# Kernel tuning notes

Measured on AMD Instinct MI355X. Metric: run time of the kernel, lower is better.

## Reference

```python
import jax, jax.numpy as jnp
import numpy as np

EMBED = 128   # embed_dim
HEADS = 8
POINTS = 4
H_SP, W_SP = 51, 102   # hardcoded spatial_shapes in __init__
BEV = 100              # bev_res
HRES = 50              # height_res


def _make_ref_points():
    """Exact numpy replica of the spherical grid built in __init__."""
    eps = 1e-6
    x = np.linspace(-71 / 2, 71 / 2, BEV)
    y = np.linspace(-71 / 2, 71 / 2, BEV)
    z = np.linspace(-50 / 2, 50 / 2, HRES)
    gx, gy, gz = np.meshgrid(x, y, z, indexing='ij')
    phi = np.sign(gy + eps) * np.arccos(gx / (np.sqrt(gx ** 2 + gy ** 2) + eps))
    theta = np.arccos(gz / (np.sqrt(gx ** 2 + gy ** 2 + gz ** 2) + eps))
    phi = 2 * np.pi - phi
    phi[phi > 2 * np.pi] -= 2 * np.pi
    col = phi / (2 * np.pi)   # grd_col_cross
    row = theta / np.pi       # grd_row_cross
    ref = np.stack([col, row], axis=-1)              # (BEV, BEV, HRES, 2)
    ref = ref.transpose(2, 0, 1, 3).reshape(HRES, BEV * BEV, 2)
    return jnp.asarray(ref, dtype=jnp.float32)


def setup_inputs() -> dict:
    key = jax.random.key(0)
    ks = jax.random.split(key, 12)
    d = EMBED
    s = 0.02
    return {
        'query': jax.random.normal(ks[0], (1, BEV * BEV, d), jnp.float32),
        'value': jax.random.normal(ks[1], (1, H_SP * W_SP, d), jnp.float32),
        'ref_points': _make_ref_points(),
        'W_off': jax.random.normal(ks[2], (d, HEADS * POINTS * 2), jnp.float32) * s,
        'b_off': jax.random.normal(ks[3], (HEADS * POINTS * 2,), jnp.float32) * s,
        'W_attn': jax.random.normal(ks[4], (d, HEADS * POINTS), jnp.float32) * s,
        'b_attn': jax.random.normal(ks[5], (HEADS * POINTS,), jnp.float32) * s,
        'W_val': jax.random.normal(ks[6], (d, d), jnp.float32) * s,
        'b_val': jax.random.normal(ks[7], (d,), jnp.float32) * s,
        'W_out': jax.random.normal(ks[8], (d, d), jnp.float32) * s,
        'b_out': jax.random.normal(ks[9], (d,), jnp.float32) * s,
        'W_proj': jax.random.normal(ks[10], (d, 1), jnp.float32) * s,
        'b_proj': jax.random.normal(ks[11], (1,), jnp.float32) * s,
    }


def _bilinear_sample(vflat, loc):
    """grid_sample(bilinear, zero padding, align_corners=False).
    vflat: (B, H*W, hd) value maps; loc: (B, N, 2) normalized [0,1] (x,y)."""
    px = loc[..., 0] * W_SP - 0.5
    py = loc[..., 1] * H_SP - 0.5
    x0 = jnp.floor(px)
    y0 = jnp.floor(py)
    dx = (px - x0)[..., None]
    dy = (py - y0)[..., None]
    x0i = x0.astype(jnp.int32)
    y0i = y0.astype(jnp.int32)

    def gather(xi, yi):
        valid = (xi >= 0) & (xi < W_SP) & (yi >= 0) & (yi < H_SP)
        idx = jnp.clip(yi, 0, H_SP - 1) * W_SP + jnp.clip(xi, 0, W_SP - 1)
        v = jnp.take_along_axis(vflat, idx[..., None], axis=1)  # (B, N, hd)
        return v * valid[..., None].astype(vflat.dtype)

    v00 = gather(x0i, y0i)
    v01 = gather(x0i + 1, y0i)
    v10 = gather(x0i, y0i + 1)
    v11 = gather(x0i + 1, y0i + 1)
    return (v00 * (1 - dx) * (1 - dy) + v01 * dx * (1 - dy)
            + v10 * (1 - dx) * dy + v11 * dx * dy)


def reference(query, value, ref_points, W_off, b_off, W_attn, b_attn,
              W_val, b_val, W_out, b_out, W_proj, b_proj):
    bs, nq, d = query.shape
    hd = d // HEADS
    L = ref_points.shape[0]

    # query-dependent MSDA projections (identical across height levels)
    offsets = (query @ W_off + b_off).reshape(bs, nq, HEADS, POINTS, 2)
    aw = jax.nn.softmax((query @ W_attn + b_attn).reshape(bs, nq, HEADS, POINTS), axis=-1)
    awt = aw.transpose(0, 2, 1, 3)                              # (bs, heads, nq, points)
    v = (value @ W_val + b_val).reshape(bs, -1, HEADS, hd)
    vflat = v.transpose(0, 2, 1, 3).reshape(bs * HEADS, H_SP * W_SP, hd)
    norm = jnp.asarray([W_SP, H_SP], dtype=query.dtype)         # offset_normalizer [W, H]

    def per_level(ref):  # ref: (nq, 2) -> MSDA output with its internal residual
        loc = ref[None, :, None, None, :] + offsets / norm      # (bs, nq, heads, pts, 2)
        loc = loc.transpose(0, 2, 1, 3, 4).reshape(bs * HEADS, nq * POINTS, 2)
        samp = _bilinear_sample(vflat, loc).reshape(bs, HEADS, nq, POINTS, hd)
        out = jnp.einsum('bhnp,bhnpd->bnhd', awt, samp).reshape(bs, nq, d)
        return out @ W_out + b_out + query                      # mmcv MSDA adds identity

    grd = jax.vmap(per_level)(ref_points)                       # (L, bs, nq, d)
    grd_3d = grd.transpose(1, 2, 0, 3).reshape(bs, BEV, BEV, L, d)
    weights = jax.nn.softmax(grd_3d @ W_proj + b_proj, axis=3)  # (bs, BEV, BEV, L, 1)
    max_height_index = jnp.argmax(weights, axis=3)              # (bs, BEV, BEV, 1)
    grd_bev = (weights * grd_3d).sum(axis=3)                    # (bs, BEV, BEV, d)
    return grd_bev.reshape(bs, nq, d) + query, max_height_index
```

## Files before the change

### kernel.cpp

```cpp
#include <hip/hip_runtime.h>
#include <math.h>

#define EMBED   128
#define NHEADS  8
#define NPOINTS 4
#define HD      16
#define HSP     51
#define WSP     102
#define NPIX    (HSP * WSP)
#define NQ      10000
#define NLVL    50

#define GRID_A ((NPIX + 7) / 8)
#define GRID_B (NQ / 8)

__global__ __launch_bounds__(256) void k_prep(
    const float* __restrict__ value,
    const float* __restrict__ Wv,
    const float* __restrict__ bv,
    const float* __restrict__ query,
    const float* __restrict__ Woff,
    const float* __restrict__ boff,
    const float* __restrict__ Wattn,
    const float* __restrict__ battn,
    const float* __restrict__ Wout,
    const float* __restrict__ Wproj,
    float* __restrict__ vout,
    float* __restrict__ off_out,
    float* __restrict__ aw_out,
    float* __restrict__ u_out) {
    const int b = blockIdx.x;
    const int t = threadIdx.x;
    __shared__ float srow[8][EMBED];

    if (b < GRID_A) {
        const int p   = t >> 5;
        const int s   = t & 31;
        const int pix = b * 8 + p;
        const int pl  = min(pix, NPIX - 1);
        *(float4*)&srow[p][s * 4] =
            *(const float4*)(value + (size_t)pl * EMBED + s * 4);
        __syncthreads();
        float4 acc = *(const float4*)(bv + s * 4);
        const float* vr = srow[p];
        const float* wp = Wv + s * 4;
#pragma unroll 8
        for (int k = 0; k < EMBED; ++k) {
            const float qv = vr[k];
            const float4 w4 = *(const float4*)(wp + (size_t)k * EMBED);
            acc.x = fmaf(qv, w4.x, acc.x);
            acc.y = fmaf(qv, w4.y, acc.y);
            acc.z = fmaf(qv, w4.z, acc.z);
            acc.w = fmaf(qv, w4.w, acc.w);
        }
        if (pix < NPIX) {
            const int h = s >> 2, c = (s & 3) * 4;
            *(float4*)(vout + ((size_t)h * NPIX + pix) * HD + c) = acc;
        }
    } else if (b < GRID_A + GRID_B) {
        const int qi = t >> 5;
        const int s  = t & 31;
        const int q  = (b - GRID_A) * 8 + qi;
        *(float4*)&srow[qi][s * 4] =
            *(const float4*)(query + (size_t)q * EMBED + s * 4);
        __syncthreads();
        if (s < 24) {
            const float* vr = srow[qi];
            const float* wp;
            int wstride;
            float4 acc;
            if (s < 16) {
                wp = Woff + s * 4; wstride = 64;
                acc = *(const float4*)(boff + s * 4);
            } else {
                wp = Wattn + (s - 16) * 4; wstride = 32;
                acc = *(const float4*)(battn + (s - 16) * 4);
            }
#pragma unroll 8
            for (int k = 0; k < EMBED; ++k) {
                const float qv = vr[k];
                const float4 w4 = *(const float4*)(wp + (size_t)k * wstride);
                acc.x = fmaf(qv, w4.x, acc.x);
                acc.y = fmaf(qv, w4.y, acc.y);
                acc.z = fmaf(qv, w4.z, acc.z);
                acc.w = fmaf(qv, w4.w, acc.w);
            }
            if (s < 16) {
                *(float4*)(off_out + (size_t)q * 64 + s * 4) = acc;
            } else {
                const float mx = fmaxf(fmaxf(acc.x, acc.y), fmaxf(acc.z, acc.w));
                const float e0 = __expf(acc.x - mx), e1 = __expf(acc.y - mx);
                const float e2 = __expf(acc.z - mx), e3 = __expf(acc.w - mx);
                const float inv = 1.f / (e0 + e1 + e2 + e3);
                float4 r;
                r.x = e0 * inv; r.y = e1 * inv; r.z = e2 * inv; r.w = e3 * inv;
                *(float4*)(aw_out + (size_t)q * 32 + (s - 16) * 4) = r;
            }
        }
    } else {
        if (t < EMBED) {
            float acc = 0.f;
#pragma unroll 8
            for (int d = 0; d < EMBED; ++d)
                acc = fmaf(Wout[(size_t)t * EMBED + d], Wproj[d], acc);
            u_out[t] = acc;
        }
    }
}

__global__ __launch_bounds__(256, 6) void k_main(
    const float* __restrict__ query,
    const float* __restrict__ refp,
    const float* __restrict__ voff,
    const float* __restrict__ vaw,
    const float* __restrict__ vflat,
    const float* __restrict__ uvec,
    const float* __restrict__ Wout,
    const float* __restrict__ bout,
    float* __restrict__ out0,
    float* __restrict__ out1) {
    const int t = threadIdx.x;
    const int qslot = t >> 7;
    const int w2 = (t >> 6) & 1;
    const int half = (t >> 5) & 1;
    const int sub = t & 31;
    const int h  = sub >> 2;
    const int c4 = sub & 3;
    const int q = blockIdx.x * 2 + qslot;

    __shared__ float  s_rpy[2][NLVL];
    __shared__ float4 s_acc[2][32];
    __shared__ float  s_z[2], s_m[2];
    __shared__ int    s_b[2];

    if (t < 2 * NLVL) {
        const int ql = t / NLVL, l = t - ql * NLVL;
        const int qq = blockIdx.x * 2 + ql;
        s_rpy[ql][l] = refp[((size_t)l * NQ + qq) * 2 + 1];
    }

    const float4* offp = (const float4*)(voff + (size_t)q * 64 + h * 8);
    const float4 o01 = offp[0];
    const float4 o23 = offp[1];
    const float4 awv4 = *(const float4*)(vaw + (size_t)q * 32 + h * 4);
    const float4 u4 = *(const float4*)(uvec + h * 16 + c4 * 4);
    const float rpx = refp[(size_t)q * 2];
    const float4* vbase = (const float4*)vflat + (size_t)h * NPIX * 4 + c4;

    const float offx[4] = {o01.x, o01.z, o23.x, o23.z};
    const float offy[4] = {o01.y, o01.w, o23.y, o23.w};
    const float awv[4]  = {awv4.x, awv4.y, awv4.z, awv4.w};

    float wx0[NPOINTS], wx1[NPOINTS], oyc[NPOINTS];
    int xo0[NPOINTS], xo1[NPOINTS];
#pragma unroll
    for (int p = 0; p < NPOINTS; ++p) {
        const float px = fmaf(rpx, (float)WSP, offx[p]) - 0.5f;
        const float fx = floorf(px);
        const float dx = px - fx;
        const int x0 = (int)fx, x1 = x0 + 1;
        const float a = awv[p];
        wx0[p] = ((unsigned)x0 < (unsigned)WSP) ? a * (1.f - dx) : 0.f;
        wx1[p] = ((unsigned)x1 < (unsigned)WSP) ? a * dx : 0.f;
        xo0[p] = min(max(x0, 0), WSP - 1) * 4;
        xo1[p] = min(max(x1, 0), WSP - 1) * 4;
        oyc[p] = offy[p] - 0.5f;
    }

    __syncthreads();

    float4 acc = {0.f, 0.f, 0.f, 0.f};
    float Z = 0.f, m = -1e30f;
    int best = 0;

#pragma unroll 1
    for (int i = 0; i < 13; ++i) {
        if (4 * i + (w2 << 1) >= NLVL) break;
        const int l = 4 * i + (w2 << 1) + half;
        const float rpy = s_rpy[qslot][l];
        float4 s = {0.f, 0.f, 0.f, 0.f};
#pragma unroll
        for (int p = 0; p < NPOINTS; ++p) {
            const float py = fmaf(rpy, (float)HSP, oyc[p]);
            const float fy = floorf(py);
            const float dy = py - fy;
            const int y0 = (int)fy, y1 = y0 + 1;
            const float t0 = ((unsigned)y0 < (unsigned)HSP) ? (1.f - dy) : 0.f;
            const float t1 = ((unsigned)y1 < (unsigned)HSP) ? dy : 0.f;
            const int rb0 = min(max(y0, 0), HSP - 1) * (WSP * 4);
            const int rb1 = min(max(y1, 0), HSP - 1) * (WSP * 4);
            const float w00 = wx0[p] * t0;
            const float w01 = wx1[p] * t0;
            const float w10 = wx0[p] * t1;
            const float w11 = wx1[p] * t1;
            const float4 v00 = vbase[rb0 + xo0[p]];
            const float4 v01 = vbase[rb0 + xo1[p]];
            const float4 v10 = vbase[rb1 + xo0[p]];
            const float4 v11 = vbase[rb1 + xo1[p]];
            s.x = fmaf(w00, v00.x, s.x); s.y = fmaf(w00, v00.y, s.y);
            s.z = fmaf(w00, v00.z, s.z); s.w = fmaf(w00, v00.w, s.w);
            s.x = fmaf(w01, v01.x, s.x); s.y = fmaf(w01, v01.y, s.y);
            s.z = fmaf(w01, v01.z, s.z); s.w = fmaf(w01, v01.w, s.w);
            s.x = fmaf(w10, v10.x, s.x); s.y = fmaf(w10, v10.y, s.y);
            s.z = fmaf(w10, v10.z, s.z); s.w = fmaf(w10, v10.w, s.w);
            s.x = fmaf(w11, v11.x, s.x); s.y = fmaf(w11, v11.y, s.y);
            s.z = fmaf(w11, v11.z, s.z); s.w = fmaf(w11, v11.w, s.w);
        }
        float part = s.x * u4.x;
        part = fmaf(s.y, u4.y, part);
        part = fmaf(s.z, u4.z, part);
        part = fmaf(s.w, u4.w, part);
#pragma unroll
        for (int d = 1; d < 32; d <<= 1)
            part += __shfl_xor(part, d, 64);
        const float e = __expf(part);
        Z += e;
        acc.x = fmaf(e, s.x, acc.x);
        acc.y = fmaf(e, s.y, acc.y);
        acc.z = fmaf(e, s.z, acc.z);
        acc.w = fmaf(e, s.w, acc.w);
        best = (part > m) ? l : best;
        m = fmaxf(part, m);
    }

    {
        const float mo = __shfl_xor(m, 32, 64);
        const int   bo = __shfl_xor(best, 32, 64);
        const float Zo = __shfl_xor(Z, 32, 64);
        const float ax = __shfl_xor(acc.x, 32, 64);
        const float ay = __shfl_xor(acc.y, 32, 64);
        const float az = __shfl_xor(acc.z, 32, 64);
        const float aw_ = __shfl_xor(acc.w, 32, 64);
        const bool takeOther = (mo > m) || (mo == m && bo < best);
        best = takeOther ? bo : best;
        m = fmaxf(m, mo);
        Z += Zo;
        acc.x += ax; acc.y += ay; acc.z += az; acc.w += aw_;
    }

    if (w2 == 1) {
        if (half == 0) s_acc[qslot][sub] = acc;
        if ((t & 63) == 0) { s_z[qslot] = Z; s_m[qslot] = m; s_b[qslot] = best; }
    }
    __syncthreads();

    if (w2 == 0) {
        const float4 ao = s_acc[qslot][sub];
        const float Zo = s_z[qslot];
        const float mo = s_m[qslot];
        const int   bo = s_b[qslot];
        const bool takeOther = (mo > m) || (mo == m && bo < best);
        best = takeOther ? bo : best;
        Z += Zo;
        acc.x += ao.x; acc.y += ao.y; acc.z += ao.z; acc.w += ao.w;

        const float inv = 1.f / Z;
        if (half == 0) {
            float4 sv;
            sv.x = acc.x * inv; sv.y = acc.y * inv;
            sv.z = acc.z * inv; sv.w = acc.w * inv;
            s_acc[qslot][sub] = sv;
            if (sub == 0) out1[q] = (float)best;
        }

        const int dpb = sub * 4;
        float4 r = {0.f, 0.f, 0.f, 0.f};
        if (half == 0) {
            const float4 b4 = *(const float4*)(bout + dpb);
            const float4 q4 = *(const float4*)(query + (size_t)q * EMBED + dpb);
            r.x = fmaf(2.f, q4.x, b4.x);
            r.y = fmaf(2.f, q4.y, b4.y);
            r.z = fmaf(2.f, q4.z, b4.z);
            r.w = fmaf(2.f, q4.w, b4.w);
        }
        const float4* srow = s_acc[qslot];
        const int cg0 = half * 16;
#pragma unroll 4
        for (int cg = cg0; cg < cg0 + 16; ++cg) {
            const float4 s4 = srow[cg];
            const float4 w0 = *(const float4*)(Wout + (size_t)(cg * 4 + 0) * EMBED + dpb);
            const float4 w1 = *(const float4*)(Wout + (size_t)(cg * 4 + 1) * EMBED + dpb);
            const float4 w2v = *(const float4*)(Wout + (size_t)(cg * 4 + 2) * EMBED + dpb);
            const float4 w3 = *(const float4*)(Wout + (size_t)(cg * 4 + 3) * EMBED + dpb);
            r.x = fmaf(s4.x, w0.x, r.x); r.y = fmaf(s4.x, w0.y, r.y);
            r.z = fmaf(s4.x, w0.z, r.z); r.w = fmaf(s4.x, w0.w, r.w);
            r.x = fmaf(s4.y, w1.x, r.x); r.y = fmaf(s4.y, w1.y, r.y);
            r.z = fmaf(s4.y, w1.z, r.z); r.w = fmaf(s4.y, w1.w, r.w);
            r.x = fmaf(s4.z, w2v.x, r.x); r.y = fmaf(s4.z, w2v.y, r.y);
            r.z = fmaf(s4.z, w2v.z, r.z); r.w = fmaf(s4.z, w2v.w, r.w);
            r.x = fmaf(s4.w, w3.x, r.x); r.y = fmaf(s4.w, w3.y, r.y);
            r.z = fmaf(s4.w, w3.z, r.z); r.w = fmaf(s4.w, w3.w, r.w);
        }
        {
            const float rx = __shfl_xor(r.x, 32, 64);
            const float ry = __shfl_xor(r.y, 32, 64);
            const float rz = __shfl_xor(r.z, 32, 64);
            const float rw = __shfl_xor(r.w, 32, 64);
            r.x += rx; r.y += ry; r.z += rz; r.w += rw;
        }
        if (half == 0)
            *(float4*)(out0 + (size_t)q * EMBED + dpb) = r;
    }
}

extern "C" void kernel_launch(void* const* d_in, const int* in_sizes, int n_in,
                              void* d_out, int out_size, void* d_ws, size_t ws_size,
                              hipStream_t stream) {
    const float* query = (const float*)d_in[0];
    const float* value = (const float*)d_in[1];
    const float* refp  = (const float*)d_in[2];
    const float* Woff  = (const float*)d_in[3];
    const float* boff  = (const float*)d_in[4];
    const float* Wattn = (const float*)d_in[5];
    const float* battn = (const float*)d_in[6];
    const float* Wval  = (const float*)d_in[7];
    const float* bval  = (const float*)d_in[8];
    const float* Wout  = (const float*)d_in[9];
    const float* bout  = (const float*)d_in[10];
    const float* Wproj = (const float*)d_in[11];

    float* ws = (float*)d_ws;
    float* ws_v   = ws;
    float* ws_off = ws_v + (size_t)NHEADS * NPIX * HD;
    float* ws_aw  = ws_off + (size_t)NQ * 64;
    float* ws_u   = ws_aw + (size_t)NQ * 32;

    float* out0 = (float*)d_out;
    float* out1 = out0 + (size_t)NQ * EMBED;

    hipLaunchKernelGGL(k_prep, dim3(GRID_A + GRID_B + 1), dim3(256), 0, stream,
                       value, Wval, bval, query, Woff, boff, Wattn, battn,
                       Wout, Wproj, ws_v, ws_off, ws_aw, ws_u);
    hipLaunchKernelGGL(k_main, dim3(NQ / 2), dim3(256), 0, stream,
                       query, refp, ws_off, ws_aw, ws_v, ws_u, Wout, bout,
                       out0, out1);
}
```

Before: 252.9 us.

## Store projected values pixel-major and batch all bilinear gathers before accumulating

The projected value tensor changes from a head-major (head, pixel, 16) layout to a pixel-major (pixel, 128) layout. All 8 heads of one query now read the same 512-byte pixel row, so each gathered corner becomes one contiguous access across the wavefront. The inner sampling loop issues all 16 float4 corner loads before doing any FMAs, to raise memory-level parallelism. Launch bounds drop from 6 to 4 waves per SIMD so the extra live registers fit, at the cost of lower occupancy.

```diff
diff --git a/kernel.cpp b/kernel.cpp
--- a/kernel.cpp
+++ b/kernel.cpp
@@ -54,8 +54,7 @@
             acc.w = fmaf(qv, w4.w, acc.w);
         }
         if (pix < NPIX) {
-            const int h = s >> 2, c = (s & 3) * 4;
-            *(float4*)(vout + ((size_t)h * NPIX + pix) * HD + c) = acc;
+            *(float4*)(vout + (size_t)pix * EMBED + s * 4) = acc;
         }
     } else if (b < GRID_A + GRID_B) {
         const int qi = t >> 5;
@@ -108,7 +107,7 @@
     }
 }
 
-__global__ __launch_bounds__(256, 6) void k_main(
+__global__ __launch_bounds__(256, 4) void k_main(
     const float* __restrict__ query,
     const float* __restrict__ refp,
     const float* __restrict__ voff,
@@ -145,7 +144,7 @@
     const float4 awv4 = *(const float4*)(vaw + (size_t)q * 32 + h * 4);
     const float4 u4 = *(const float4*)(uvec + h * 16 + c4 * 4);
     const float rpx = refp[(size_t)q * 2];
-    const float4* vbase = (const float4*)vflat + (size_t)h * NPIX * 4 + c4;
+    const float4* vbase = (const float4*)vflat + h * 4 + c4;
 
     const float offx[4] = {o01.x, o01.z, o23.x, o23.z};
     const float offy[4] = {o01.y, o01.w, o23.y, o23.w};
@@ -162,8 +161,8 @@
         const float a = awv[p];
         wx0[p] = ((unsigned)x0 < (unsigned)WSP) ? a * (1.f - dx) : 0.f;
         wx1[p] = ((unsigned)x1 < (unsigned)WSP) ? a * dx : 0.f;
-        xo0[p] = min(max(x0, 0), WSP - 1) * 4;
-        xo1[p] = min(max(x1, 0), WSP - 1) * 4;
+        xo0[p] = min(max(x0, 0), WSP - 1) * 32;
+        xo1[p] = min(max(x1, 0), WSP - 1) * 32;
         oyc[p] = offy[p] - 0.5f;
     }
 
@@ -178,7 +177,9 @@
         if (4 * i + (w2 << 1) >= NLVL) break;
         const int l = 4 * i + (w2 << 1) + half;
         const float rpy = s_rpy[qslot][l];
-        float4 s = {0.f, 0.f, 0.f, 0.f};
+
+        float4 v00[NPOINTS], v01[NPOINTS], v10[NPOINTS], v11[NPOINTS];
+        float w00[NPOINTS], w01[NPOINTS], w10[NPOINTS], w11[NPOINTS];
 #pragma unroll
         for (int p = 0; p < NPOINTS; ++p) {
             const float py = fmaf(rpy, (float)HSP, oyc[p]);
@@ -187,24 +188,28 @@
             const int y0 = (int)fy, y1 = y0 + 1;
             const float t0 = ((unsigned)y0 < (unsigned)HSP) ? (1.f - dy) : 0.f;
             const float t1 = ((unsigned)y1 < (unsigned)HSP) ? dy : 0.f;
-            const int rb0 = min(max(y0, 0), HSP - 1) * (WSP * 4);
-            const int rb1 = min(max(y1, 0), HSP - 1) * (WSP * 4);
-            const float w00 = wx0[p] * t0;
-            const float w01 = wx1[p] * t0;
-            const float w10 = wx0[p] * t1;
-            const float w11 = wx1[p] * t1;
-            const float4 v00 = vbase[rb0 + xo0[p]];
-            const float4 v01 = vbase[rb0 + xo1[p]];
-            const float4 v10 = vbase[rb1 + xo0[p]];
-            const float4 v11 = vbase[rb1 + xo1[p]];
-            s.x = fmaf(w00, v00.x, s.x); s.y = fmaf(w00, v00.y, s.y);
-            s.z = fmaf(w00, v00.z, s.z); s.w = fmaf(w00, v00.w, s.w);
-            s.x = fmaf(w01, v01.x, s.x); s.y = fmaf(w01, v01.y, s.y);
-            s.z = fmaf(w01, v01.z, s.z); s.w = fmaf(w01, v01.w, s.w);
-            s.x = fmaf(w10, v10.x, s.x); s.y = fmaf(w10, v10.y, s.y);
-            s.z = fmaf(w10, v10.z, s.z); s.w = fmaf(w10, v10.w, s.w);
-            s.x = fmaf(w11, v11.x, s.x); s.y = fmaf(w11, v11.y, s.y);
-            s.z = fmaf(w11, v11.z, s.z); s.w = fmaf(w11, v11.w, s.w);
+            const int rb0 = min(max(y0, 0), HSP - 1) * (WSP * 32);
+            const int rb1 = min(max(y1, 0), HSP - 1) * (WSP * 32);
+            v00[p] = vbase[rb0 + xo0[p]];
+            v01[p] = vbase[rb0 + xo1[p]];
+            v10[p] = vbase[rb1 + xo0[p]];
+            v11[p] = vbase[rb1 + xo1[p]];
+            w00[p] = wx0[p] * t0;
+            w01[p] = wx1[p] * t0;
+            w10[p] = wx0[p] * t1;
+            w11[p] = wx1[p] * t1;
+        }
+        float4 s = {0.f, 0.f, 0.f, 0.f};
+#pragma unroll
+        for (int p = 0; p < NPOINTS; ++p) {
+            s.x = fmaf(w00[p], v00[p].x, s.x); s.y = fmaf(w00[p], v00[p].y, s.y);
+            s.z = fmaf(w00[p], v00[p].z, s.z); s.w = fmaf(w00[p], v00[p].w, s.w);
+            s.x = fmaf(w01[p], v01[p].x, s.x); s.y = fmaf(w01[p], v01[p].y, s.y);
+            s.z = fmaf(w01[p], v01[p].z, s.z); s.w = fmaf(w01[p], v01[p].w, s.w);
+            s.x = fmaf(w10[p], v10[p].x, s.x); s.y = fmaf(w10[p], v10[p].y, s.y);
+            s.z = fmaf(w10[p], v10[p].z, s.z); s.w = fmaf(w10[p], v10[p].w, s.w);
+            s.x = fmaf(w11[p], v11[p].x, s.x); s.y = fmaf(w11[p], v11[p].y, s.y);
+            s.z = fmaf(w11[p], v11[p].z, s.z); s.w = fmaf(w11[p], v11[p].w, s.w);
         }
         float part = s.x * u4.x;
         part = fmaf(s.y, u4.y, part);
@@ -321,7 +326,7 @@
 
     float* ws = (float*)d_ws;
     float* ws_v   = ws;
-    float* ws_off = ws_v + (size_t)NHEADS * NPIX * HD;
+    float* ws_off = ws_v + (size_t)NPIX * EMBED;
     float* ws_aw  = ws_off + (size_t)NQ * 64;
     float* ws_u   = ws_aw + (size_t)NQ * 32;
 
```

Measured after the change: 250.5 us. About the same (-0.9%).
